# Performance work log

Measured on AMD Instinct MI355X. Metric: run time of the kernel, lower is better.

Reference implementation:

```python
import jax, jax.numpy as jnp
import numpy as np

L, B, H, E, V = 64, 2048, 1024, 50, 256  # seq_len, batch, hidden, char_emb, char_vocab
PAD = 0


def setup_inputs() -> dict:
    key = jax.random.key(0)
    ks = jax.random.split(key, 10)
    s = 1.0 / np.sqrt(H)  # torch LSTM default init scale
    emb = jax.random.normal(ks[0], (V, E), jnp.float32)
    emb = emb.at[PAD].set(0.0)  # padding_idx row
    return {
        "input": jax.random.randint(ks[1], (L, B), 0, V, jnp.int32),
        "h0": jax.random.normal(ks[2], (1, B, H), jnp.float32),
        "c0": jax.random.normal(ks[3], (1, B, H), jnp.float32),
        "emb": emb,
        "W_ih": jax.random.uniform(ks[4], (4 * H, E), jnp.float32, -s, s),
        "W_hh": jax.random.uniform(ks[5], (4 * H, H), jnp.float32, -s, s),
        "b_ih": jax.random.uniform(ks[6], (4 * H,), jnp.float32, -s, s),
        "b_hh": jax.random.uniform(ks[7], (4 * H,), jnp.float32, -s, s),
        "W_proj": jax.random.uniform(ks[8], (V, H), jnp.float32, -s, s),
        "b_proj": jax.random.uniform(ks[9], (V,), jnp.float32, -s, s),
    }


def reference(input, h0, c0, emb, W_ih, W_hh, b_ih, b_hh, W_proj, b_proj):
    # char embedding lookup: (L, B, E)
    x = emb[input]
    b = b_ih + b_hh

    def step(carry, x_t):
        h, c = carry  # (B, H) each
        gates = x_t @ W_ih.T + h @ W_hh.T + b  # (B, 4H), torch gate order i,f,g,o
        i, f, g, o = jnp.split(gates, 4, axis=-1)
        c_new = jax.nn.sigmoid(f) * c + jax.nn.sigmoid(i) * jnp.tanh(g)
        h_new = jax.nn.sigmoid(o) * jnp.tanh(c_new)
        return (h_new, c_new), h_new

    (hT, cT), hs = jax.lax.scan(step, (h0[0], c0[0]), x)
    # per-step linear projection of hidden state (same math as looped Linear)
    scores = hs @ W_proj.T + b_proj  # (L, B, V)
    return scores, hT[None], cT[None]
```

## Files before the change

kernel.cpp:

```cpp
#include <hip/hip_runtime.h>
#include <hip/hip_bf16.h>
#include <cstdint>
#include <cstddef>

#define LSEQ  64
#define BATCH 2048
#define HID   1024
#define NGATE 4096
#define VOC   256
#define EMBD  50

using bf16 = __hip_bfloat16;
typedef __attribute__((ext_vector_type(8))) __bf16 bf16x8;
typedef __attribute__((ext_vector_type(4))) float  f32x4;

__device__ __forceinline__ void gload_lds16(const void* g, void* l) {
  __builtin_amdgcn_global_load_lds(
      (const __attribute__((address_space(1))) unsigned int*)g,
      (__attribute__((address_space(3))) unsigned int*)l, 16, 0, 0);
}

__device__ __forceinline__ float sigf(float x) {
  x = fminf(fmaxf(x, -30.f), 30.f);
  return 1.f / (1.f + __expf(-x));
}
__device__ __forceinline__ float tanh_f(float x) {
  x = fminf(fmaxf(x, -15.f), 15.f);
  float e = __expf(2.f * x);
  return (e - 1.f) / (e + 1.f);
}


__global__ void k_prep_whh(const float* __restrict__ W, bf16* __restrict__ Wr) {
  size_t i = (size_t)blockIdx.x * 256 + threadIdx.x;
  int k  = (int)(i & 1023);
  int np = (int)(i >> 10);
  int T = np >> 7, w = np & 127;
  int wc = w >> 6, g = (w >> 4) & 3, hl = w & 15;
  int grow = g * HID + T * 32 + wc * 16 + hl;
  Wr[i] = __float2bfloat16(W[(size_t)grow * HID + k]);
}

__global__ void k_prep_embw(const float* __restrict__ emb, const float* __restrict__ W_ih,
                            const float* __restrict__ b_ih, const float* __restrict__ b_hh,
                            float* __restrict__ embW) {
  size_t i = (size_t)blockIdx.x * 256 + threadIdx.x;
  int np = (int)(i & 4095);
  int v  = (int)(i >> 12);
  int T = np >> 7, w = np & 127;
  int wc = w >> 6, g = (w >> 4) & 3, hl = w & 15;
  int grow = g * HID + T * 32 + wc * 16 + hl;
  float s = b_ih[grow] + b_hh[grow];
  #pragma unroll 10
  for (int e = 0; e < EMBD; ++e)
    s += emb[(size_t)v * EMBD + e] * W_ih[(size_t)grow * EMBD + e];
  embW[i] = s;
}

__global__ void k_prep_wp(const float* __restrict__ Wp_f, bf16* __restrict__ Wp) {
  size_t i = (size_t)blockIdx.x * 256 + threadIdx.x;
  Wp[i] = __float2bfloat16(Wp_f[i]);
}

__global__ void k_init_state(const float* __restrict__ h0, const float* __restrict__ c0,
                             bf16* __restrict__ h, float* __restrict__ c) {
  size_t i = (size_t)blockIdx.x * 256 + threadIdx.x;
  h[i] = __float2bfloat16(h0[i]);
  c[i] = c0[i];
}

template<int MODE>
__global__ __launch_bounds__(512) void g8(
    const bf16* __restrict__ Abase, const bf16* __restrict__ Bbase,
    const float* __restrict__ c_in, float* __restrict__ c_out,
    bf16* __restrict__ h_out,
    const float* __restrict__ embW, const int* __restrict__ input,
    const float* __restrict__ b_proj, float* __restrict__ out,
    int t, int kc, int nslots)
{
  __shared__ __align__(16) bf16 lsA[3 * 256 * 64];
  __shared__ __align__(16) bf16 lsB[3 * 128 * 64];

  const int tid  = threadIdx.x;
  const int wave = tid >> 6, lane = tid & 63;
  const int wr = wave >> 1, wc = wave & 1;
  const int hl = lane & 15, q = lane >> 4;

  int bx, by;
  if constexpr (MODE == 0) {
    int id = blockIdx.x, xcd = id & 7, idx = id >> 3;
    by = xcd + ((idx & 3) << 3);
    bx = idx >> 2;
  } else {
    bx = blockIdx.x; by = blockIdx.y;
  }

  const bf16* Asrc;
  if constexpr (MODE == 0) {
    Asrc = Abase + (size_t)bx * 256 * HID;
  } else {
    int t_local = bx >> 3;
    int slot = (kc + 1 + t_local) % nslots;
    Asrc = Abase + ((size_t)slot * BATCH + (size_t)(bx & 7) * 256) * HID;
  }
  const bf16* Bsrc = Bbase + (size_t)by * 128 * HID;

  const bf16 *pA0, *pA1, *pA2, *pA3, *pB0, *pB1;
  {
    int g0 = tid,      r0 = g0 >> 3, c0v = (g0 & 7) ^ (r0 & 7);
    int g1 = 512+tid,  r1 = g1 >> 3, c1v = (g1 & 7) ^ (r1 & 7);
    int g2 = 1024+tid, r2 = g2 >> 3, c2v = (g2 & 7) ^ (r2 & 7);
    int g3 = 1536+tid, r3 = g3 >> 3, c3v = (g3 & 7) ^ (r3 & 7);
    pA0 = Asrc + (size_t)r0 * HID + c0v * 8;
    pA1 = Asrc + (size_t)r1 * HID + c1v * 8;
    pA2 = Asrc + (size_t)r2 * HID + c2v * 8;
    pA3 = Asrc + (size_t)r3 * HID + c3v * 8;
    pB0 = Bsrc + (size_t)r0 * HID + c0v * 8;
    pB1 = Bsrc + (size_t)r1 * HID + c1v * 8;
  }
  bf16* dA = lsA + wave * 512;
  bf16* dB = lsB + wave * 512;

  int aofs0[4], aofs1[4], bofs0[4], bofs1[4];
  #pragma unroll
  for (int m = 0; m < 4; ++m) {
    int row = wr * 64 + m * 16 + hl;
    aofs0[m] = row * 64 + ((q ^ (hl & 7)) * 8);
    aofs1[m] = row * 64 + (((4 + q) ^ (hl & 7)) * 8);
  }
  #pragma unroll
  for (int n = 0; n < 4; ++n) {
    int row = wc * 64 + n * 16 + hl;
    bofs0[n] = row * 64 + ((q ^ (hl & 7)) * 8);
    bofs1[n] = row * 64 + (((4 + q) ^ (hl & 7)) * 8);
  }

  f32x4 acc[4][4] = {};

#define STG_P0(S_) { gload_lds16(pA0, dA + (S_)*16384);         pA0 += 64;  \
                     gload_lds16(pA1, dA + (S_)*16384 + 4096);  pA1 += 64;  \
                     gload_lds16(pA2, dA + (S_)*16384 + 8192);  pA2 += 64; }
#define STG_P1(S_) { gload_lds16(pA3, dA + (S_)*16384 + 12288); pA3 += 64;  \
                     gload_lds16(pB0, dB + (S_)*8192);          pB0 += 64;  \
                     gload_lds16(pB1, dB + (S_)*8192 + 4096);   pB1 += 64; }

#define PHASE(Ab_, Bb_, AO_, BO_, STG_) {                                   \
    bf16x8 aF[4], bF[4];                                                    \
    _Pragma("unroll")                                                       \
    for (int m = 0; m < 4; ++m) aF[m] = *(const bf16x8*)((Ab_) + AO_[m]);   \
    _Pragma("unroll")                                                       \
    for (int n = 0; n < 4; ++n) bF[n] = *(const bf16x8*)((Bb_) + BO_[n]);   \
    STG_;                                                                   \
    __builtin_amdgcn_s_barrier();                                           \
    asm volatile("s_waitcnt lgkmcnt(0)" ::: "memory");                      \
    __builtin_amdgcn_sched_barrier(0);                                      \
    __builtin_amdgcn_s_setprio(1);                                          \
    _Pragma("unroll")                                                       \
    for (int m = 0; m < 4; ++m)                                             \
      _Pragma("unroll")                                                     \
      for (int n = 0; n < 4; ++n)                                           \
        acc[m][n] = __builtin_amdgcn_mfma_f32_16x16x32_bf16(aF[m], bF[n], acc[m][n], 0, 0, 0); \
    __builtin_amdgcn_s_setprio(0);                                          \
  }

  STG_P0(0); STG_P1(0);
  STG_P0(1); STG_P1(1);
  __builtin_amdgcn_sched_barrier(0);

  int cur = 0, st = 2;
  for (int T = 0; T < 15; ++T) {
    asm volatile("s_waitcnt vmcnt(6)" ::: "memory");
    __builtin_amdgcn_s_barrier();
    const bf16* Ab = lsA + cur * 16384;
    const bf16* Bb = lsB + cur * 8192;
    if (T < 14) {
      PHASE(Ab, Bb, aofs0, bofs0, STG_P0(st));
      PHASE(Ab, Bb, aofs1, bofs1, STG_P1(st));
    } else {
      PHASE(Ab, Bb, aofs0, bofs0, );
      PHASE(Ab, Bb, aofs1, bofs1, );
    }
    cur = (cur == 2) ? 0 : cur + 1;
    st  = (st  == 2) ? 0 : st  + 1;
  }
  asm volatile("s_waitcnt vmcnt(0)" ::: "memory");
  __builtin_amdgcn_s_barrier();
  {
    const bf16* Ab = lsA + cur * 16384;
    const bf16* Bb = lsB + cur * 8192;
    PHASE(Ab, Bb, aofs0, bofs0, );
    PHASE(Ab, Bb, aofs1, bofs1, );
  }
  __builtin_amdgcn_sched_barrier(0);

#undef STG_P0
#undef STG_P1
#undef PHASE

  const int qrow = q * 4;

  if constexpr (MODE == 0) {
    const int h_idx = by * 32 + wc * 16 + hl;
    const float* ewc = embW + (size_t)(by * 128 + wc * 64);
    #pragma unroll
    for (int m = 0; m < 4; ++m) {
      const int b0 = bx * 256 + wr * 64 + m * 16 + qrow;
      const int4 iv = *(const int4*)(input + (size_t)t * BATCH + b0);
      #pragma unroll
      for (int r = 0; r < 4; ++r) {
        const int idx = (&iv.x)[r];
        const float* ew = ewc + (size_t)idx * NGATE;
        float ivv = acc[m][0][r] + ew[hl];
        float fv  = acc[m][1][r] + ew[16 + hl];
        float gv  = acc[m][2][r] + ew[32 + hl];
        float ov  = acc[m][3][r] + ew[48 + hl];
        const size_t off = (size_t)(b0 + r) * HID + h_idx;
        float cn = sigf(fv) * c_in[off] + sigf(ivv) * tanh_f(gv);
        float hn = sigf(ov) * tanh_f(cn);
        h_out[off] = __float2bfloat16(hn);
        c_out[off] = cn;
        if (t == LSEQ - 1) {
          out[(size_t)LSEQ * BATCH * VOC + off] = hn;
          out[(size_t)LSEQ * BATCH * VOC + (size_t)BATCH * HID + off] = cn;
        }
      }
    }
  } else {
    const int t_glob = kc + (bx >> 3);
    float* os = out + (size_t)t_glob * BATCH * VOC;
    const int b0base = (bx & 7) * 256 + wr * 64;
    #pragma unroll
    for (int m = 0; m < 4; ++m) {
      #pragma unroll
      for (int n = 0; n < 4; ++n) {
        const int v = by * 128 + wc * 64 + n * 16 + hl;
        const float bp = b_proj[v];
        #pragma unroll
        for (int r = 0; r < 4; ++r)
          os[(size_t)(b0base + m * 16 + qrow + r) * VOC + v] = acc[m][n][r] + bp;
      }
    }
  }
}


extern "C" void kernel_launch(void* const* d_in, const int* in_sizes, int n_in,
                              void* d_out, int out_size, void* d_ws, size_t ws_size,
                              hipStream_t stream)
{
  (void)in_sizes; (void)n_in; (void)out_size;
  const int*   input  = (const int*)  d_in[0];
  const float* h0     = (const float*)d_in[1];
  const float* c0     = (const float*)d_in[2];
  const float* emb    = (const float*)d_in[3];
  const float* W_ih   = (const float*)d_in[4];
  const float* W_hh   = (const float*)d_in[5];
  const float* b_ih   = (const float*)d_in[6];
  const float* b_hh   = (const float*)d_in[7];
  const float* W_proj = (const float*)d_in[8];
  const float* b_proj = (const float*)d_in[9];
  float* out = (float*)d_out;

  char* ws = (char*)d_ws;
  bf16*  Wr   = (bf16*)(ws);
  bf16*  Wp   = (bf16*)(ws + 8388608);
  float* embW = (float*)(ws + 8912896);
  float* cb0  = (float*)(ws + 13107200);
  float* cb1  = (float*)(ws + 21495808);
  bf16*  hs   = (bf16*)(ws + 29884416);
  const size_t fixed = 29884416;
  const size_t slotB = (size_t)BATCH * HID * sizeof(bf16);

  int nslots = 2;
  const int cand[6] = {65, 17, 9, 5, 3, 2};
  for (int i = 0; i < 6; ++i)
    if (fixed + (size_t)cand[i] * slotB <= ws_size) { nslots = cand[i]; break; }
  const int chunk = nslots - 1;

  k_prep_whh <<<16384, 256, 0, stream>>>(W_hh, Wr);
  k_prep_wp  <<<1024,  256, 0, stream>>>(W_proj, Wp);
  k_prep_embw<<<4096,  256, 0, stream>>>(emb, W_ih, b_ih, b_hh, embW);
  k_init_state<<<8192, 256, 0, stream>>>(h0, c0, hs, cb0);

  float* cbuf[2] = {cb0, cb1};
  for (int kc = 0; kc < LSEQ; kc += chunk) {
    for (int t = kc; t < kc + chunk; ++t) {
      const int si = t % nslots, so = (t + 1) % nslots;
      g8<0><<<dim3(256), 512, 0, stream>>>(
          hs + (size_t)si * BATCH * HID, Wr,
          cbuf[t & 1], cbuf[(t + 1) & 1],
          hs + (size_t)so * BATCH * HID,
          embW, input, b_proj, out, t, 0, 0);
    }
    g8<1><<<dim3(8 * chunk, 2), 512, 0, stream>>>(
        hs, Wp, nullptr, nullptr, nullptr,
        nullptr, nullptr, b_proj, out, 0, kc, nslots);
  }
}
```

Before: 1.888 ms.

## Replace per-step LSTM kernel launches with persistent kernel using atomic flag sync

Folds the 64 per-timestep recurrent GEMM launches into one persistent kernel of 256 blocks. Each block keeps its cell state in registers and waits on per-batch-tile atomic counters, so it only needs the 32 blocks that produce its own batch rows rather than a full grid barrier. The projection GEMM then runs once over all 64 stored hidden states. This removes launch overhead and the c-state round trips through global memory. It assumes all 256 blocks are resident at the same time, uses a bounded spin-wait, and hardcodes 65 h slots with no check of workspace size.

New measurement: 4.965 ms. 2.63x slower.

```diff
diff --git a/kernel.cpp b/kernel.cpp
--- a/kernel.cpp
+++ b/kernel.cpp
@@ -62,21 +62,18 @@
   Wp[i] = __float2bfloat16(Wp_f[i]);
 }
 
-__global__ void k_init_state(const float* __restrict__ h0, const float* __restrict__ c0,
-                             bf16* __restrict__ h, float* __restrict__ c) {
+__global__ void k_init_state(const float* __restrict__ h0, bf16* __restrict__ hs,
+                             int* __restrict__ arr) {
   size_t i = (size_t)blockIdx.x * 256 + threadIdx.x;
-  h[i] = __float2bfloat16(h0[i]);
-  c[i] = c0[i];
-}
-
-template<int MODE>
-__global__ __launch_bounds__(512) void g8(
-    const bf16* __restrict__ Abase, const bf16* __restrict__ Bbase,
-    const float* __restrict__ c_in, float* __restrict__ c_out,
-    bf16* __restrict__ h_out,
+  hs[i] = __float2bfloat16(h0[i]);
+  if (i < 520) arr[i] = 0;
+}
+
+__global__ __launch_bounds__(512) void g_persist(
+    const float* __restrict__ c0, const bf16* __restrict__ Wr,
+    bf16* __restrict__ hs, int* __restrict__ arr,
     const float* __restrict__ embW, const int* __restrict__ input,
-    const float* __restrict__ b_proj, float* __restrict__ out,
-    int t, int kc, int nslots)
+    float* __restrict__ out, int nslots)
 {
   __shared__ __align__(16) bf16 lsA[3 * 256 * 64];
   __shared__ __align__(16) bf16 lsB[3 * 128 * 64];
@@ -86,23 +83,180 @@
   const int wr = wave >> 1, wc = wave & 1;
   const int hl = lane & 15, q = lane >> 4;
 
-  int bx, by;
-  if constexpr (MODE == 0) {
-    int id = blockIdx.x, xcd = id & 7, idx = id >> 3;
-    by = xcd + ((idx & 3) << 3);
-    bx = idx >> 2;
-  } else {
-    bx = blockIdx.x; by = blockIdx.y;
-  }
-
-  const bf16* Asrc;
-  if constexpr (MODE == 0) {
-    Asrc = Abase + (size_t)bx * 256 * HID;
-  } else {
-    int t_local = bx >> 3;
-    int slot = (kc + 1 + t_local) % nslots;
-    Asrc = Abase + ((size_t)slot * BATCH + (size_t)(bx & 7) * 256) * HID;
-  }
+  const int bx = blockIdx.x & 7;
+  const int by = blockIdx.x >> 3;
+  const int bxbase = bx * 256;
+
+  const bf16* Bsrc = Wr + (size_t)by * 128 * HID;
+
+  size_t offA0, offA1, offA2, offA3;
+  {
+    int g0 = tid,      r0 = g0 >> 3, c0v = (g0 & 7) ^ (r0 & 7);
+    int g1 = 512+tid,  r1 = g1 >> 3, c1v = (g1 & 7) ^ (r1 & 7);
+    int g2 = 1024+tid, r2 = g2 >> 3, c2v = (g2 & 7) ^ (r2 & 7);
+    int g3 = 1536+tid, r3 = g3 >> 3, c3v = (g3 & 7) ^ (r3 & 7);
+    offA0 = (size_t)r0 * HID + c0v * 8;
+    offA1 = (size_t)r1 * HID + c1v * 8;
+    offA2 = (size_t)r2 * HID + c2v * 8;
+    offA3 = (size_t)r3 * HID + c3v * 8;
+  }
+  bf16* dA = lsA + wave * 512;
+  bf16* dB = lsB + wave * 512;
+
+  int aofs0[4], aofs1[4], bofs0[4], bofs1[4];
+  #pragma unroll
+  for (int m = 0; m < 4; ++m) {
+    int row = wr * 64 + m * 16 + hl;
+    aofs0[m] = row * 64 + ((q ^ (hl & 7)) * 8);
+    aofs1[m] = row * 64 + (((4 + q) ^ (hl & 7)) * 8);
+  }
+  #pragma unroll
+  for (int n = 0; n < 4; ++n) {
+    int row = wc * 64 + n * 16 + hl;
+    bofs0[n] = row * 64 + ((q ^ (hl & 7)) * 8);
+    bofs1[n] = row * 64 + (((4 + q) ^ (hl & 7)) * 8);
+  }
+
+  const int h_idx = by * 32 + wc * 16 + hl;
+  float creg[4][4];
+  #pragma unroll
+  for (int m = 0; m < 4; ++m)
+    #pragma unroll
+    for (int r = 0; r < 4; ++r)
+      creg[m][r] = c0[(size_t)(bxbase + wr * 64 + m * 16 + q * 4 + r) * HID + h_idx];
+
+  const float* ewc = embW + (size_t)(by * 128 + wc * 64);
+  const size_t slotE = (size_t)BATCH * HID;
+
+#define SSTG0(S_) { gload_lds16(pA0, dA + (S_)*16384);         pA0 += 64;  \
+                    gload_lds16(pA1, dA + (S_)*16384 + 4096);  pA1 += 64;  \
+                    gload_lds16(pA2, dA + (S_)*16384 + 8192);  pA2 += 64; }
+#define SSTG1(S_) { gload_lds16(pA3, dA + (S_)*16384 + 12288); pA3 += 64;  \
+                    gload_lds16(pB0, dB + (S_)*8192);          pB0 += 64;  \
+                    gload_lds16(pB1, dB + (S_)*8192 + 4096);   pB1 += 64; }
+
+#define SPHASE(Ab_, Bb_, AO_, BO_, STG_) {                                  \
+    bf16x8 aF[4], bF[4];                                                    \
+    _Pragma("unroll")                                                       \
+    for (int m = 0; m < 4; ++m) aF[m] = *(const bf16x8*)((Ab_) + AO_[m]);   \
+    _Pragma("unroll")                                                       \
+    for (int n = 0; n < 4; ++n) bF[n] = *(const bf16x8*)((Bb_) + BO_[n]);   \
+    STG_;                                                                   \
+    __builtin_amdgcn_s_barrier();                                           \
+    asm volatile("s_waitcnt lgkmcnt(0)" ::: "memory");                      \
+    __builtin_amdgcn_sched_barrier(0);                                      \
+    __builtin_amdgcn_s_setprio(1);                                          \
+    _Pragma("unroll")                                                       \
+    for (int m = 0; m < 4; ++m)                                             \
+      _Pragma("unroll")                                                     \
+      for (int n = 0; n < 4; ++n)                                           \
+        acc[m][n] = __builtin_amdgcn_mfma_f32_16x16x32_bf16(aF[m], bF[n], acc[m][n], 0, 0, 0); \
+    __builtin_amdgcn_s_setprio(0);                                          \
+  }
+
+  for (int t = 0; t < LSEQ; ++t) {
+    if (t) {
+      if (tid == 0) {
+        int it = 0;
+        while (__hip_atomic_load(&arr[t * 8 + bx], __ATOMIC_ACQUIRE,
+                                 __HIP_MEMORY_SCOPE_AGENT) < 32 && ++it < (1 << 20))
+          __builtin_amdgcn_s_sleep(2);
+      }
+      __syncthreads();
+    }
+
+    const bf16* Asrc = hs + (size_t)(t % nslots) * slotE + (size_t)bxbase * HID;
+    const bf16 *pA0 = Asrc + offA0, *pA1 = Asrc + offA1;
+    const bf16 *pA2 = Asrc + offA2, *pA3 = Asrc + offA3;
+    const bf16 *pB0 = Bsrc + offA0, *pB1 = Bsrc + offA1;
+
+    f32x4 acc[4][4] = {};
+
+    SSTG0(0); SSTG1(0);
+    SSTG0(1); SSTG1(1);
+    __builtin_amdgcn_sched_barrier(0);
+
+    int cur = 0, st = 2;
+    for (int T = 0; T < 15; ++T) {
+      asm volatile("s_waitcnt vmcnt(6)" ::: "memory");
+      __builtin_amdgcn_s_barrier();
+      const bf16* Ab = lsA + cur * 16384;
+      const bf16* Bb = lsB + cur * 8192;
+      if (T < 14) {
+        SPHASE(Ab, Bb, aofs0, bofs0, SSTG0(st));
+        SPHASE(Ab, Bb, aofs1, bofs1, SSTG1(st));
+      } else {
+        SPHASE(Ab, Bb, aofs0, bofs0, );
+        SPHASE(Ab, Bb, aofs1, bofs1, );
+      }
+      cur = (cur == 2) ? 0 : cur + 1;
+      st  = (st  == 2) ? 0 : st  + 1;
+    }
+    asm volatile("s_waitcnt vmcnt(0)" ::: "memory");
+    __builtin_amdgcn_s_barrier();
+    {
+      const bf16* Ab = lsA + cur * 16384;
+      const bf16* Bb = lsB + cur * 8192;
+      SPHASE(Ab, Bb, aofs0, bofs0, );
+      SPHASE(Ab, Bb, aofs1, bofs1, );
+    }
+    __builtin_amdgcn_sched_barrier(0);
+
+    bf16* hout = hs + (size_t)((t + 1) % nslots) * slotE;
+    #pragma unroll
+    for (int m = 0; m < 4; ++m) {
+      const int b0 = bxbase + wr * 64 + m * 16 + q * 4;
+      const int4 iv = *(const int4*)(input + (size_t)t * BATCH + b0);
+      #pragma unroll
+      for (int r = 0; r < 4; ++r) {
+        const int idx = (&iv.x)[r];
+        const float* ew = ewc + (size_t)idx * NGATE;
+        float gi = acc[m][0][r] + ew[hl];
+        float gf = acc[m][1][r] + ew[16 + hl];
+        float gg = acc[m][2][r] + ew[32 + hl];
+        float go = acc[m][3][r] + ew[48 + hl];
+        float cn = sigf(gf) * creg[m][r] + sigf(gi) * tanh_f(gg);
+        float hn = sigf(go) * tanh_f(cn);
+        creg[m][r] = cn;
+        const size_t off = (size_t)(b0 + r) * HID + h_idx;
+        hout[off] = __float2bfloat16(hn);
+        if (t == LSEQ - 1) {
+          out[(size_t)LSEQ * BATCH * VOC + off] = hn;
+          out[(size_t)LSEQ * BATCH * VOC + slotE + off] = cn;
+        }
+      }
+    }
+
+    __threadfence();
+    __syncthreads();
+    if (tid == 0)
+      __hip_atomic_fetch_add(&arr[(t + 1) * 8 + bx], 1, __ATOMIC_RELEASE,
+                             __HIP_MEMORY_SCOPE_AGENT);
+  }
+#undef SSTG0
+#undef SSTG1
+#undef SPHASE
+}
+
+template<int MODE>
+__global__ __launch_bounds__(512) void g8(
+    const bf16* __restrict__ Abase, const bf16* __restrict__ Bbase,
+    const float* __restrict__ b_proj, float* __restrict__ out,
+    int kc, int nslots)
+{
+  __shared__ __align__(16) bf16 lsA[3 * 256 * 64];
+  __shared__ __align__(16) bf16 lsB[3 * 128 * 64];
+
+  const int tid  = threadIdx.x;
+  const int wave = tid >> 6, lane = tid & 63;
+  const int wr = wave >> 1, wc = wave & 1;
+  const int hl = lane & 15, q = lane >> 4;
+
+  const int bx = blockIdx.x, by = blockIdx.y;
+
+  int t_local = bx >> 3;
+  int slot = (kc + 1 + t_local) % nslots;
+  const bf16* Asrc = Abase + ((size_t)slot * BATCH + (size_t)(bx & 7) * 256) * HID;
   const bf16* Bsrc = Bbase + (size_t)by * 128 * HID;
 
   const bf16 *pA0, *pA1, *pA2, *pA3, *pB0, *pB1;
@@ -191,54 +345,24 @@
     PHASE(Ab, Bb, aofs0, bofs0, );
     PHASE(Ab, Bb, aofs1, bofs1, );
   }
-  __builtin_amdgcn_sched_barrier(0);
 
 #undef STG_P0
 #undef STG_P1
 #undef PHASE
 
   const int qrow = q * 4;
-
-  if constexpr (MODE == 0) {
-    const int h_idx = by * 32 + wc * 16 + hl;
-    const float* ewc = embW + (size_t)(by * 128 + wc * 64);
+  const int t_glob = kc + (bx >> 3);
+  float* os = out + (size_t)t_glob * BATCH * VOC;
+  const int b0base = (bx & 7) * 256 + wr * 64;
+  #pragma unroll
+  for (int m = 0; m < 4; ++m) {
     #pragma unroll
-    for (int m = 0; m < 4; ++m) {
-      const int b0 = bx * 256 + wr * 64 + m * 16 + qrow;
-      const int4 iv = *(const int4*)(input + (size_t)t * BATCH + b0);
+    for (int n = 0; n < 4; ++n) {
+      const int v = by * 128 + wc * 64 + n * 16 + hl;
+      const float bp = b_proj[v];
       #pragma unroll
-      for (int r = 0; r < 4; ++r) {
-        const int idx = (&iv.x)[r];
-        const float* ew = ewc + (size_t)idx * NGATE;
-        float ivv = acc[m][0][r] + ew[hl];
-        float fv  = acc[m][1][r] + ew[16 + hl];
-        float gv  = acc[m][2][r] + ew[32 + hl];
-        float ov  = acc[m][3][r] + ew[48 + hl];
-        const size_t off = (size_t)(b0 + r) * HID + h_idx;
-        float cn = sigf(fv) * c_in[off] + sigf(ivv) * tanh_f(gv);
-        float hn = sigf(ov) * tanh_f(cn);
-        h_out[off] = __float2bfloat16(hn);
-        c_out[off] = cn;
-        if (t == LSEQ - 1) {
-          out[(size_t)LSEQ * BATCH * VOC + off] = hn;
-          out[(size_t)LSEQ * BATCH * VOC + (size_t)BATCH * HID + off] = cn;
-        }
-      }
-    }
-  } else {
-    const int t_glob = kc + (bx >> 3);
-    float* os = out + (size_t)t_glob * BATCH * VOC;
-    const int b0base = (bx & 7) * 256 + wr * 64;
-    #pragma unroll
-    for (int m = 0; m < 4; ++m) {
-      #pragma unroll
-      for (int n = 0; n < 4; ++n) {
-        const int v = by * 128 + wc * 64 + n * 16 + hl;
-        const float bp = b_proj[v];
-        #pragma unroll
-        for (int r = 0; r < 4; ++r)
-          os[(size_t)(b0base + m * 16 + qrow + r) * VOC + v] = acc[m][n][r] + bp;
-      }
+      for (int r = 0; r < 4; ++r)
+        os[(size_t)(b0base + m * 16 + qrow + r) * VOC + v] = acc[m][n][r] + bp;
     }
   }
 }
@@ -248,7 +372,7 @@
                               void* d_out, int out_size, void* d_ws, size_t ws_size,
                               hipStream_t stream)
 {
-  (void)in_sizes; (void)n_in; (void)out_size;
+  (void)in_sizes; (void)n_in; (void)out_size; (void)ws_size;
   const int*   input  = (const int*)  d_in[0];
   const float* h0     = (const float*)d_in[1];
   const float* c0     = (const float*)d_in[2];
@@ -265,35 +389,16 @@
   bf16*  Wr   = (bf16*)(ws);
   bf16*  Wp   = (bf16*)(ws + 8388608);
   float* embW = (float*)(ws + 8912896);
-  float* cb0  = (float*)(ws + 13107200);
-  float* cb1  = (float*)(ws + 21495808);
-  bf16*  hs   = (bf16*)(ws + 29884416);
-  const size_t fixed = 29884416;
-  const size_t slotB = (size_t)BATCH * HID * sizeof(bf16);
-
-  int nslots = 2;
-  const int cand[6] = {65, 17, 9, 5, 3, 2};
-  for (int i = 0; i < 6; ++i)
-    if (fixed + (size_t)cand[i] * slotB <= ws_size) { nslots = cand[i]; break; }
-  const int chunk = nslots - 1;
+  int*   arr  = (int*)  (ws + 13107200);
+  bf16*  hs   = (bf16*) (ws + 13111296);
+  const int nslots = 65;
 
   k_prep_whh <<<16384, 256, 0, stream>>>(W_hh, Wr);
   k_prep_wp  <<<1024,  256, 0, stream>>>(W_proj, Wp);
   k_prep_embw<<<4096,  256, 0, stream>>>(emb, W_ih, b_ih, b_hh, embW);
-  k_init_state<<<8192, 256, 0, stream>>>(h0, c0, hs, cb0);
-
-  float* cbuf[2] = {cb0, cb1};
-  for (int kc = 0; kc < LSEQ; kc += chunk) {
-    for (int t = kc; t < kc + chunk; ++t) {
-      const int si = t % nslots, so = (t + 1) % nslots;
-      g8<0><<<dim3(256), 512, 0, stream>>>(
-          hs + (size_t)si * BATCH * HID, Wr,
-          cbuf[t & 1], cbuf[(t + 1) & 1],
-          hs + (size_t)so * BATCH * HID,
-          embW, input, b_proj, out, t, 0, 0);
-    }
-    g8<1><<<dim3(8 * chunk, 2), 512, 0, stream>>>(
-        hs, Wp, nullptr, nullptr, nullptr,
-        nullptr, nullptr, b_proj, out, 0, kc, nslots);
-  }
-}
+  k_init_state<<<8192, 256, 0, stream>>>(h0, hs, arr);
+
+  g_persist<<<dim3(256), 512, 0, stream>>>(c0, Wr, hs, arr, embW, input, out, nslots);
+
+  g8<1><<<dim3(8 * 64, 2), 512, 0, stream>>>(hs, Wp, b_proj, out, 0, nslots);
+}
```

## Restructure GEMM k-loop to one barrier per tile and interleave embW gates

Applied to the files above, without the earlier changes.

The GEMM main loop now issues all six async global-to-LDS copies for a stage at once. It loads both k-halves of the fragments, then runs 32 MFMAs, with only one wait and barrier per k-tile instead of two. The loop is manually unrolled by three so the ring-buffer slot indices are compile-time constants. The embedding-times-W_ih table is re-laid out with the four gates interleaved, so the LSTM epilogue fetches them with one float4 load instead of four scattered loads. The slot count is also hardcoded to 65 with a projection chunk of 16, which ignores ws_size and could overflow a smaller workspace.

Result: no change. 1.893 ms (+0.3%).

```diff
diff --git a/kernel.cpp b/kernel.cpp
--- a/kernel.cpp
+++ b/kernel.cpp
@@ -45,11 +45,10 @@
                             const float* __restrict__ b_ih, const float* __restrict__ b_hh,
                             float* __restrict__ embW) {
   size_t i = (size_t)blockIdx.x * 256 + threadIdx.x;
-  int np = (int)(i & 4095);
-  int v  = (int)(i >> 12);
-  int T = np >> 7, w = np & 127;
-  int wc = w >> 6, g = (w >> 4) & 3, hl = w & 15;
-  int grow = g * HID + T * 32 + wc * 16 + hl;
+  int v     = (int)(i >> 12);
+  int h_col = (int)((i >> 2) & 1023);
+  int g     = (int)(i & 3);
+  int grow = g * HID + h_col;
   float s = b_ih[grow] + b_hh[grow];
   #pragma unroll 10
   for (int e = 0; e < EMBD; ++e)
@@ -63,10 +62,10 @@
 }
 
 __global__ void k_init_state(const float* __restrict__ h0, const float* __restrict__ c0,
-                             bf16* __restrict__ h, float* __restrict__ c) {
-  size_t i = (size_t)blockIdx.x * 256 + threadIdx.x;
-  h[i] = __float2bfloat16(h0[i]);
-  c[i] = c0[i];
+                             bf16* __restrict__ hs, float* __restrict__ cb) {
+  size_t i = (size_t)blockIdx.x * 256 + threadIdx.x;
+  hs[i] = __float2bfloat16(h0[i]);
+  cb[i] = c0[i];
 }
 
 template<int MODE>
@@ -137,71 +136,68 @@
 
   f32x4 acc[4][4] = {};
 
-#define STG_P0(S_) { gload_lds16(pA0, dA + (S_)*16384);         pA0 += 64;  \
-                     gload_lds16(pA1, dA + (S_)*16384 + 4096);  pA1 += 64;  \
-                     gload_lds16(pA2, dA + (S_)*16384 + 8192);  pA2 += 64; }
-#define STG_P1(S_) { gload_lds16(pA3, dA + (S_)*16384 + 12288); pA3 += 64;  \
-                     gload_lds16(pB0, dB + (S_)*8192);          pB0 += 64;  \
-                     gload_lds16(pB1, dB + (S_)*8192 + 4096);   pB1 += 64; }
-
-#define PHASE(Ab_, Bb_, AO_, BO_, STG_) {                                   \
-    bf16x8 aF[4], bF[4];                                                    \
-    _Pragma("unroll")                                                       \
-    for (int m = 0; m < 4; ++m) aF[m] = *(const bf16x8*)((Ab_) + AO_[m]);   \
-    _Pragma("unroll")                                                       \
-    for (int n = 0; n < 4; ++n) bF[n] = *(const bf16x8*)((Bb_) + BO_[n]);   \
-    STG_;                                                                   \
-    __builtin_amdgcn_s_barrier();                                           \
-    asm volatile("s_waitcnt lgkmcnt(0)" ::: "memory");                      \
+#define STG6(S_) { gload_lds16(pA0, dA + (S_)*16384);         pA0 += 64;  \
+                   gload_lds16(pA1, dA + (S_)*16384 + 4096);  pA1 += 64;  \
+                   gload_lds16(pA2, dA + (S_)*16384 + 8192);  pA2 += 64;  \
+                   gload_lds16(pA3, dA + (S_)*16384 + 12288); pA3 += 64;  \
+                   gload_lds16(pB0, dB + (S_)*8192);          pB0 += 64;  \
+                   gload_lds16(pB1, dB + (S_)*8192 + 4096);   pB1 += 64; }
+
+#define KTILE(S_, DOST_, ST_) {                                             \
+    const bf16* Ab = lsA + (S_) * 16384;                                    \
+    const bf16* Bb = lsB + (S_) * 8192;                                     \
+    if (DOST_) STG6(ST_);                                                   \
+    bf16x8 a0[4], b0[4], a1[4], b1[4];                                      \
+    _Pragma("unroll")                                                       \
+    for (int m = 0; m < 4; ++m) { a0[m] = *(const bf16x8*)(Ab + aofs0[m]);  \
+                                  a1[m] = *(const bf16x8*)(Ab + aofs1[m]); }\
+    _Pragma("unroll")                                                       \
+    for (int n = 0; n < 4; ++n) { b0[n] = *(const bf16x8*)(Bb + bofs0[n]);  \
+                                  b1[n] = *(const bf16x8*)(Bb + bofs1[n]); }\
     __builtin_amdgcn_sched_barrier(0);                                      \
     __builtin_amdgcn_s_setprio(1);                                          \
     _Pragma("unroll")                                                       \
     for (int m = 0; m < 4; ++m)                                             \
       _Pragma("unroll")                                                     \
       for (int n = 0; n < 4; ++n)                                           \
-        acc[m][n] = __builtin_amdgcn_mfma_f32_16x16x32_bf16(aF[m], bF[n], acc[m][n], 0, 0, 0); \
+        acc[m][n] = __builtin_amdgcn_mfma_f32_16x16x32_bf16(a0[m], b0[n], acc[m][n], 0, 0, 0); \
     __builtin_amdgcn_s_setprio(0);                                          \
-  }
-
-  STG_P0(0); STG_P1(0);
-  STG_P0(1); STG_P1(1);
+    __builtin_amdgcn_sched_barrier(0);                                      \
+    __builtin_amdgcn_s_setprio(1);                                          \
+    _Pragma("unroll")                                                       \
+    for (int m = 0; m < 4; ++m)                                             \
+      _Pragma("unroll")                                                     \
+      for (int n = 0; n < 4; ++n)                                           \
+        acc[m][n] = __builtin_amdgcn_mfma_f32_16x16x32_bf16(a1[m], b1[n], acc[m][n], 0, 0, 0); \
+    __builtin_amdgcn_s_setprio(0);                                          \
+  }
+
+#define WAIT6 { asm volatile("s_waitcnt vmcnt(6)" ::: "memory"); __builtin_amdgcn_s_barrier(); }
+
+  STG6(0); STG6(1);
   __builtin_amdgcn_sched_barrier(0);
 
-  int cur = 0, st = 2;
-  for (int T = 0; T < 15; ++T) {
-    asm volatile("s_waitcnt vmcnt(6)" ::: "memory");
-    __builtin_amdgcn_s_barrier();
-    const bf16* Ab = lsA + cur * 16384;
-    const bf16* Bb = lsB + cur * 8192;
-    if (T < 14) {
-      PHASE(Ab, Bb, aofs0, bofs0, STG_P0(st));
-      PHASE(Ab, Bb, aofs1, bofs1, STG_P1(st));
-    } else {
-      PHASE(Ab, Bb, aofs0, bofs0, );
-      PHASE(Ab, Bb, aofs1, bofs1, );
-    }
-    cur = (cur == 2) ? 0 : cur + 1;
-    st  = (st  == 2) ? 0 : st  + 1;
-  }
-  asm volatile("s_waitcnt vmcnt(0)" ::: "memory");
-  __builtin_amdgcn_s_barrier();
-  {
-    const bf16* Ab = lsA + cur * 16384;
-    const bf16* Bb = lsB + cur * 8192;
-    PHASE(Ab, Bb, aofs0, bofs0, );
-    PHASE(Ab, Bb, aofs1, bofs1, );
-  }
+  #pragma unroll 1
+  for (int Tq = 0; Tq < 4; ++Tq) {
+    WAIT6; KTILE(0, 1, 2);
+    WAIT6; KTILE(1, 1, 0);
+    WAIT6; KTILE(2, 1, 1);
+  }
+  WAIT6; KTILE(0, 1, 2);
+  WAIT6; KTILE(1, 1, 0);
+  WAIT6; KTILE(2, 0, 0);
+  { asm volatile("s_waitcnt vmcnt(0)" ::: "memory"); __builtin_amdgcn_s_barrier(); }
+  KTILE(0, 0, 0);
   __builtin_amdgcn_sched_barrier(0);
 
-#undef STG_P0
-#undef STG_P1
-#undef PHASE
+#undef STG6
+#undef KTILE
+#undef WAIT6
 
   const int qrow = q * 4;
 
   if constexpr (MODE == 0) {
     const int h_idx = by * 32 + wc * 16 + hl;
-    const float* ewc = embW + (size_t)(by * 128 + wc * 64);
     #pragma unroll
     for (int m = 0; m < 4; ++m) {
       const int b0 = bx * 256 + wr * 64 + m * 16 + qrow;
@@ -209,14 +205,14 @@
       #pragma unroll
       for (int r = 0; r < 4; ++r) {
         const int idx = (&iv.x)[r];
-        const float* ew = ewc + (size_t)idx * NGATE;
-        float ivv = acc[m][0][r] + ew[hl];
-        float fv  = acc[m][1][r] + ew[16 + hl];
-        float gv  = acc[m][2][r] + ew[32 + hl];
-        float ov  = acc[m][3][r] + ew[48 + hl];
+        const float4 e = *(const float4*)(embW + ((size_t)idx * 1024 + h_idx) * 4);
+        float gi = acc[m][0][r] + e.x;
+        float gf = acc[m][1][r] + e.y;
+        float gg = acc[m][2][r] + e.z;
+        float go = acc[m][3][r] + e.w;
         const size_t off = (size_t)(b0 + r) * HID + h_idx;
-        float cn = sigf(fv) * c_in[off] + sigf(ivv) * tanh_f(gv);
-        float hn = sigf(ov) * tanh_f(cn);
+        float cn = sigf(gf) * c_in[off] + sigf(gi) * tanh_f(gg);
+        float hn = sigf(go) * tanh_f(cn);
         h_out[off] = __float2bfloat16(hn);
         c_out[off] = cn;
         if (t == LSEQ - 1) {
@@ -248,7 +244,7 @@
                               void* d_out, int out_size, void* d_ws, size_t ws_size,
                               hipStream_t stream)
 {
-  (void)in_sizes; (void)n_in; (void)out_size;
+  (void)in_sizes; (void)n_in; (void)out_size; (void)ws_size;
   const int*   input  = (const int*)  d_in[0];
   const float* h0     = (const float*)d_in[1];
   const float* c0     = (const float*)d_in[2];
@@ -267,15 +263,9 @@
   float* embW = (float*)(ws + 8912896);
   float* cb0  = (float*)(ws + 13107200);
   float* cb1  = (float*)(ws + 21495808);
-  bf16*  hs   = (bf16*)(ws + 29884416);
-  const size_t fixed = 29884416;
-  const size_t slotB = (size_t)BATCH * HID * sizeof(bf16);
-
-  int nslots = 2;
-  const int cand[6] = {65, 17, 9, 5, 3, 2};
-  for (int i = 0; i < 6; ++i)
-    if (fixed + (size_t)cand[i] * slotB <= ws_size) { nslots = cand[i]; break; }
-  const int chunk = nslots - 1;
+  bf16*  hs   = (bf16*) (ws + 29884416);
+  const int nslots = 65;
+  const int chunk  = 16;
 
   k_prep_whh <<<16384, 256, 0, stream>>>(W_hh, Wr);
   k_prep_wp  <<<1024,  256, 0, stream>>>(W_proj, Wp);
@@ -285,11 +275,10 @@
   float* cbuf[2] = {cb0, cb1};
   for (int kc = 0; kc < LSEQ; kc += chunk) {
     for (int t = kc; t < kc + chunk; ++t) {
-      const int si = t % nslots, so = (t + 1) % nslots;
       g8<0><<<dim3(256), 512, 0, stream>>>(
-          hs + (size_t)si * BATCH * HID, Wr,
+          hs + (size_t)(t % nslots) * BATCH * HID, Wr,
           cbuf[t & 1], cbuf[(t + 1) & 1],
-          hs + (size_t)so * BATCH * HID,
+          hs + (size_t)((t + 1) % nslots) * BATCH * HID,
           embW, input, b_proj, out, t, 0, 0);
     }
     g8<1><<<dim3(8 * chunk, 2), 512, 0, stream>>>(
```
